# Performance work log

Measured on AMD Instinct MI355X. Metric: run time of the kernel, lower is better.

## Reference

```python
import jax, jax.numpy as jnp
import numpy as np

VOC = 32000; D = 512; DFF = 2048; L = 4; H = 8; DH = D // H
NN = 256; K = 8; NB = 32; R = 128; SMAX = 1024; B = 4; S = 1024
STD = 0.02


def _ln(x, s, b):
    m = x.mean(-1, keepdims=True)
    v = ((x - m) ** 2).mean(-1, keepdims=True)
    return (x - m) / jnp.sqrt(v + 1e-5) * s + b


def setup_inputs() -> dict:
    key = jax.random.key(0)
    ks = jax.random.split(key, 24)
    p = {}
    p["input_ids"] = jax.random.randint(ks[0], (B, S), 0, VOC)
    p["token_emb"] = jax.random.normal(ks[1], (VOC, D)) * STD
    p["pos_emb"] = jax.random.normal(ks[2], (SMAX, D)) * STD
    # fixed shared basis buffers (orthogonalized at init in torch; random stand-in, same forward math)
    bA = jax.random.normal(ks[3], (NB, D, R))
    p["basis_A"] = bA / jnp.linalg.norm(bA.reshape(NB, -1), axis=-1)[:, None, None]
    be = jax.random.normal(ks[4], (NB, D))
    p["basis_emb"] = be / jnp.linalg.norm(be, axis=-1, keepdims=True)
    # per-layer params stacked on leading L axis; torch Linear weight is [out, in]
    p["q_w"] = jax.random.normal(ks[5], (L, D, D)) * STD
    p["q_b"] = jnp.zeros((L, D))
    p["k_w"] = jax.random.normal(ks[6], (L, D, D)) * STD
    p["k_b"] = jnp.zeros((L, D))
    p["ao_w"] = jax.random.normal(ks[7], (L, D, D)) * STD
    p["ao_b"] = jnp.zeros((L, D))
    p["recipe"] = jax.random.normal(ks[8], (L, NN, NB)) * 0.5
    p["ctx_pat"] = jax.random.normal(ks[9], (L, NN, H)) * 0.5
    p["vout_w"] = jax.random.normal(ks[10], (L, D, R)) * STD
    p["vout_b"] = jnp.zeros((L, D))
    p["up_w"] = jax.random.normal(ks[11], (L, DFF, D)) * STD
    p["up_b"] = jnp.zeros((L, DFF))
    p["down_w"] = jax.random.normal(ks[12], (L, D, DFF)) * STD
    p["down_b"] = jnp.zeros((L, D))
    p["ln1_s"] = jnp.ones((L, D)); p["ln1_b"] = jnp.zeros((L, D))
    p["ln2_s"] = jnp.ones((L, D)); p["ln2_b"] = jnp.zeros((L, D))
    p["lnf_s"] = jnp.ones((D,)); p["lnf_b"] = jnp.zeros((D,))
    return p


def reference(input_ids, token_emb, pos_emb, basis_A, basis_emb,
              q_w, q_b, k_w, k_b, ao_w, ao_b, recipe, ctx_pat,
              vout_w, vout_b, up_w, up_b, down_w, down_b,
              ln1_s, ln1_b, ln2_s, ln2_b, lnf_s, lnf_b):
    Bb, Ss = input_ids.shape
    x = token_emb[input_ids] + pos_emb[:Ss][None]  # [B,S,D]
    causal = jnp.tril(jnp.ones((Ss, Ss), dtype=bool))
    scale = 1.0 / np.sqrt(DH)
    for l in range(L):
        normed = _ln(x, ln1_s[l], ln1_b[l])
        Q = (normed @ q_w[l].T + q_b[l]).reshape(Bb, Ss, H, DH).transpose(0, 2, 1, 3)
        Kk = (normed @ k_w[l].T + k_b[l]).reshape(Bb, Ss, H, DH).transpose(0, 2, 1, 3)
        scores = jnp.einsum('bhsd,bhtd->bhst', Q, Kk) * scale
        scores = jnp.where(causal, scores, -jnp.inf)
        attn = jax.nn.softmax(scores, axis=-1)  # [B,H,S,S]
        # --- neuron-based dynamic V ---
        rec_sm = jax.nn.softmax(recipe[l], axis=-1)        # [NN,NB]
        emb_sem = rec_sm @ basis_emb                        # [NN,D]
        sem = normed @ emb_sem.T                            # [B,S,NN]
        summary = attn.mean(-1).transpose(0, 2, 1)          # [B,S,H]
        ctx = summary @ ctx_pat[l].T                        # [B,S,NN]
        fin = sem * jax.nn.sigmoid(ctx)
        topv, idx = jax.lax.top_k(fin, K)                   # [B,S,K]
        w = jax.nn.softmax(topv, axis=-1)
        sel = jax.nn.softmax(recipe[l][idx], axis=-1)       # [B,S,K,NB]
        token_recipe = jnp.einsum('bskn,bsk->bsn', sel, w)  # [B,S,NB]
        # reassociated contraction (same math as bsn,ndr->bsdr then bsd,bsdr->bsr)
        xA = jnp.einsum('bsd,ndr->bsnr', normed, basis_A)   # [B,S,NB,R]
        v_sem = jnp.einsum('bsn,bsnr->bsr', token_recipe, xA)
        Vv = (v_sem @ vout_w[l].T + vout_b[l]).reshape(Bb, Ss, H, DH).transpose(0, 2, 1, 3)
        ao = jnp.einsum('bhst,bhtd->bhsd', attn, Vv).transpose(0, 2, 1, 3).reshape(Bb, Ss, D)
        x = x + ao @ ao_w[l].T + ao_b[l]
        normed2 = _ln(x, ln2_s[l], ln2_b[l])
        h = jax.nn.gelu(normed2 @ up_w[l].T + up_b[l], approximate=False)
        x = x + h @ down_w[l].T + down_b[l]
    x = _ln(x, lnf_s, lnf_b)
    return x @ token_emb.T  # tied head, [B,S,vocab]
```

## Files before the change

kernel.cpp:

```cpp
#include <hip/hip_runtime.h>
#include <hip/hip_bf16.h>
#include <math.h>

typedef __attribute__((ext_vector_type(8))) short short8;
typedef __attribute__((ext_vector_type(4))) short short4v;
typedef __attribute__((ext_vector_type(8))) __bf16 bf16x8;
typedef __attribute__((ext_vector_type(4))) float f32x4;
typedef unsigned short ushort;

#define DEVI static __device__ __forceinline__

DEVI ushort f2bf(float f) {
  union { float f; unsigned u; } v; v.f = f;
  unsigned r = v.u + 0x7fffu + ((v.u >> 16) & 1u);
  return (ushort)(r >> 16);
}
DEVI float bf2f(ushort h) {
  union { unsigned u; float f; } v; v.u = (unsigned)h << 16; return v.f;
}
DEVI void gload16(const void* g, void* l) {
  __builtin_amdgcn_global_load_lds((const __attribute__((address_space(1))) void*)g,
                                   (__attribute__((address_space(3))) void*)l, 16, 0, 0);
}

template<int BM, int EPI>
__global__ __launch_bounds__(256) void gemmT(
    const ushort* __restrict__ A, const ushort* __restrict__ B,
    void* __restrict__ Cv, const float* __restrict__ bias,
    int K, int lda, int ldb, int ldc, float scale)
{
  constexpr int MF = BM / 32;
  constexpr int MH = BM / 2;
  __shared__ ushort As[BM * 32];
  __shared__ ushort Bs[4096];

  const int gx = gridDim.x;
  const int nwg = gx * gridDim.y;
  const int orig = blockIdx.y * gx + blockIdx.x;
  const int q = nwg >> 3, r = nwg & 7;
  const int xcd = orig & 7, sidx = orig >> 3;
  const int wg = (xcd < r ? xcd * (q + 1) : r * (q + 1) + (xcd - r) * q) + sidx;
  const int n0 = (wg % gx) * 128, m0 = (wg / gx) * BM;

  const int tid = threadIdx.x;
  const int arow = tid >> 2, acolb = (tid & 3) << 4;
  const int lane = tid & 63, wv = tid >> 6;
  const int wm = wv >> 1, wn = wv & 1;
  const int l16 = lane & 15, lq = lane >> 4;

  f32x4 acc[MF][4];
#pragma unroll
  for (int i = 0; i < MF; i++)
#pragma unroll
    for (int j = 0; j < 4; j++) acc[i][j] = (f32x4){0.f, 0.f, 0.f, 0.f};

  const char* Ab = (const char*)(A + (long)(m0 + arow) * lda) + acolb;
  const char* Bb = (const char*)(B + (long)(n0 + arow) * ldb) + acolb;
  const long a64 = (long)64 * lda * 2, b64 = (long)64 * ldb * 2;
  char* la = (char*)As + tid * 16;
  char* lb = (char*)Bs + tid * 16;

  for (int k0 = 0; k0 < K; k0 += 32) {
    const char* ap = Ab + (long)k0 * 2;
    const char* bp = Bb + (long)k0 * 2;
#pragma unroll
    for (int s = 0; s < BM / 64; s++) gload16(ap + s * a64, la + s * 4096);
    gload16(bp, lb);
    gload16(bp + b64, lb + 4096);
    __syncthreads();
    bf16x8 af[MF], bfr[4];
#pragma unroll
    for (int i = 0; i < MF; i++)
      af[i] = __builtin_bit_cast(bf16x8, *(const short8*)&As[(wm*MH + i*16 + l16)*32 + lq*8]);
#pragma unroll
    for (int j = 0; j < 4; j++)
      bfr[j] = __builtin_bit_cast(bf16x8, *(const short8*)&Bs[(wn*64 + j*16 + l16)*32 + lq*8]);
#pragma unroll
    for (int i = 0; i < MF; i++)
#pragma unroll
      for (int j = 0; j < 4; j++)
        acc[i][j] = __builtin_amdgcn_mfma_f32_16x16x32_bf16(af[i], bfr[j], acc[i][j], 0, 0, 0);
    __syncthreads();
  }

  float* Cf = (float*)Cv;
  ushort* Ch = (ushort*)Cv;
#pragma unroll
  for (int i = 0; i < MF; i++) {
    const int row0 = m0 + wm*MH + i*16 + lq*4;
#pragma unroll
    for (int j = 0; j < 4; j++) {
      const int col = n0 + wn*64 + j*16 + l16;
      const float cb = bias ? bias[col] : 0.f;
#pragma unroll
      for (int t = 0; t < 4; t++) {
        float val = acc[i][j][t] * scale + cb;
        const long idx = (long)(row0 + t) * ldc + col;
        if (EPI == 1)      Ch[idx] = f2bf(val);
        else if (EPI == 2) { val = 0.5f * val * (1.f + erff(val * 0.70710678118654752f)); Ch[idx] = f2bf(val); }
        else if (EPI == 3) Cf[idx] += val;
        else               __builtin_nontemporal_store(val, Cf + idx);
      }
    }
  }
}

__global__ __launch_bounds__(256) void megag1(
    const ushort* __restrict__ A, const ushort* __restrict__ B,
    float* __restrict__ finb, ushort* __restrict__ qkh, ushort* __restrict__ XAb,
    const float* __restrict__ gate, const float* __restrict__ qkbias)
{
  __shared__ ushort As[4096];
  __shared__ ushort Bs[4096];
  const int gx = gridDim.x;
  const int nwg = gx * gridDim.y;
  const int orig = blockIdx.y * gx + blockIdx.x;
  const int q = nwg >> 3, r = nwg & 7;
  const int xcd = orig & 7, sidx = orig >> 3;
  const int wg = (xcd < r ? xcd * (q + 1) : r * (q + 1) + (xcd - r) * q) + sidx;
  const int n0 = (wg % gx) * 128, m0 = (wg / gx) * 128;

  const int tid = threadIdx.x;
  const int arow = tid >> 2, acolb = (tid & 3) << 4;
  const int lane = tid & 63, wv = tid >> 6;
  const int wm = wv >> 1, wn = wv & 1;
  const int l16 = lane & 15, lq = lane >> 4;

  f32x4 acc[4][4];
#pragma unroll
  for (int i = 0; i < 4; i++)
#pragma unroll
    for (int j = 0; j < 4; j++) acc[i][j] = (f32x4){0.f, 0.f, 0.f, 0.f};

  const char* Ab = (const char*)(A + (long)(m0 + arow) * 512) + acolb;
  const char* Bb = (const char*)(B + (long)(n0 + arow) * 512) + acolb;
  const long a64 = (long)64 * 512 * 2;
  char* la = (char*)As + tid * 16;
  char* lb = (char*)Bs + tid * 16;

  for (int k0 = 0; k0 < 512; k0 += 32) {
    const char* ap = Ab + (long)k0 * 2;
    const char* bp = Bb + (long)k0 * 2;
    gload16(ap, la);
    gload16(ap + a64, la + 4096);
    gload16(bp, lb);
    gload16(bp + a64, lb + 4096);
    __syncthreads();
    bf16x8 af[4], bfr[4];
#pragma unroll
    for (int i = 0; i < 4; i++) {
      af[i]  = __builtin_bit_cast(bf16x8, *(const short8*)&As[(wm*64 + i*16 + l16)*32 + lq*8]);
      bfr[i] = __builtin_bit_cast(bf16x8, *(const short8*)&Bs[(wn*64 + i*16 + l16)*32 + lq*8]);
    }
#pragma unroll
    for (int i = 0; i < 4; i++)
#pragma unroll
      for (int j = 0; j < 4; j++)
        acc[i][j] = __builtin_amdgcn_mfma_f32_16x16x32_bf16(af[i], bfr[j], acc[i][j], 0, 0, 0);
    __syncthreads();
  }

#pragma unroll
  for (int i = 0; i < 4; i++) {
    const int row0 = m0 + wm*64 + i*16 + lq*4;
#pragma unroll
    for (int j = 0; j < 4; j++) {
      const int col = n0 + wn*64 + j*16 + l16;
      if (col < 256) {
        const float g = gate[col];
#pragma unroll
        for (int t = 0; t < 4; t++) finb[(long)(row0 + t) * 256 + col] = acc[i][j][t] * g;
      } else if (col < 1280) {
        const int c = col - 256;
        const float bb = qkbias[c];
#pragma unroll
        for (int t = 0; t < 4; t++) qkh[(long)(row0 + t) * 1024 + c] = f2bf(acc[i][j][t] + bb);
      } else {
        const int c = col - 1280;
#pragma unroll
        for (int t = 0; t < 4; t++) XAb[(long)(row0 + t) * 4096 + c] = f2bf(acc[i][j][t]);
      }
    }
  }
}

__global__ __launch_bounds__(256) void flash_kernel(
    const ushort* __restrict__ qk, const ushort* __restrict__ v,
    ushort* __restrict__ o)
{
  __shared__ ushort Ks[4096];
  __shared__ ushort VTs[4096];
  __shared__ ushort Ps[4096];
  const int p = blockIdx.x, bh = blockIdx.y;
  const int b = bh >> 3, h = bh & 7;
  const int tid = threadIdx.x, lane = tid & 63, w = tid >> 6;
  const int l16 = lane & 15, lq = lane >> 4;
  const long tokbase = (long)b * 1024;
  const ushort* Qbase = qk + tokbase * 1024 + h * 64;
  const char*   Kbase = (const char*)(qk + tokbase * 1024 + 512 + h * 64);
  const ushort* Vbase = v + tokbase * 512 + h * 64;

  const int krow = tid >> 3, kcb = (tid & 7) << 4;
  const int vkv  = tid >> 2, vdb = (tid & 3) << 4;

#pragma unroll 1
  for (int half = 0; half < 2; half++) {
    const int qt = half ? (15 - p) : p;
    const int q0 = qt * 64;
    const int ntiles = qt + 1;

    const ushort* qrow = Qbase + (long)(q0 + w*16 + l16) * 1024;
    const bf16x8 qf0 = *(const bf16x8*)(qrow + lq*8);
    const bf16x8 qf1 = *(const bf16x8*)(qrow + 32 + lq*8);

    float m_[4] = {-1e30f, -1e30f, -1e30f, -1e30f};
    float l_[4] = {0.f, 0.f, 0.f, 0.f};
    f32x4 od[4];
#pragma unroll
    for (int dt = 0; dt < 4; dt++) od[dt] = (f32x4){0.f, 0.f, 0.f, 0.f};

#pragma unroll 1
    for (int t = 0; t < ntiles; t++) {
      const long t0 = (long)t * 64;
      {
        const int swz = kcb ^ ((krow & 7) << 4);
        gload16(Kbase + (t0 + krow) * 2048 + swz, (char*)Ks + tid * 16);
        gload16(Kbase + (t0 + 32 + krow) * 2048 + swz, (char*)Ks + 4096 + tid * 16);
      }
      {
        const ushort* vr = Vbase + (t0 + vkv) * 512 + vdb;
        short8 va = *(const short8*)vr;
        short8 vb = *(const short8*)(vr + 8);
#pragma unroll
        for (int j = 0; j < 8; j++) {
          int d1 = vdb + j, d2 = vdb + 8 + j;
          *(ushort*)((char*)VTs + d1*128 + ((vkv*2) ^ ((d1 & 7) << 4))) = (ushort)va[j];
          *(ushort*)((char*)VTs + d2*128 + ((vkv*2) ^ ((d2 & 7) << 4))) = (ushort)vb[j];
        }
      }
      __syncthreads();

      f32x4 sa[4];
#pragma unroll
      for (int n = 0; n < 4; n++) sa[n] = (f32x4){0.f, 0.f, 0.f, 0.f};
#pragma unroll
      for (int ks = 0; ks < 2; ks++) {
        const bf16x8 qf = ks ? qf1 : qf0;
#pragma unroll
        for (int n = 0; n < 4; n++) {
          const int row = n*16 + l16;
          bf16x8 kf = *(const bf16x8*)((const char*)Ks + row*128 + ((ks*64 + lq*16) ^ ((row & 7) << 4)));
          sa[n] = __builtin_amdgcn_mfma_f32_16x16x32_bf16(qf, kf, sa[n], 0, 0, 0);
        }
      }

      const bool diag = (t == qt);
      float rowmax[4] = {-1e30f, -1e30f, -1e30f, -1e30f};
#pragma unroll
      for (int n = 0; n < 4; n++)
#pragma unroll
        for (int r = 0; r < 4; r++) {
          float sv = sa[n][r] * 0.125f;
          if (diag && (n*16 + l16 > w*16 + lq*4 + r)) sv = -1e30f;
          sa[n][r] = sv;
          rowmax[r] = fmaxf(rowmax[r], sv);
        }
#pragma unroll
      for (int r = 0; r < 4; r++)
#pragma unroll
        for (int off = 8; off; off >>= 1) rowmax[r] = fmaxf(rowmax[r], __shfl_xor(rowmax[r], off));

      float psum[4];
#pragma unroll
      for (int r = 0; r < 4; r++) {
        const float mn = fmaxf(m_[r], rowmax[r]);
        const float corr = __expf(m_[r] - mn);
        m_[r] = mn;
        l_[r] *= corr;
#pragma unroll
        for (int dt = 0; dt < 4; dt++) od[dt][r] *= corr;
        psum[r] = 0.f;
      }
#pragma unroll
      for (int n = 0; n < 4; n++)
#pragma unroll
        for (int r = 0; r < 4; r++) {
          const float pv = __expf(sa[n][r] - m_[r]);
          psum[r] += pv;
          const int prow = w*16 + lq*4 + r;
          *(ushort*)((char*)Ps + prow*128 + (((n*16 + l16)*2) ^ ((prow & 7) << 4))) = f2bf(pv);
        }
#pragma unroll
      for (int r = 0; r < 4; r++) {
#pragma unroll
        for (int off = 8; off; off >>= 1) psum[r] += __shfl_xor(psum[r], off);
        l_[r] += psum[r];
      }

#pragma unroll
      for (int ks = 0; ks < 2; ks++) {
        const int prow = w*16 + l16;
        bf16x8 pf = *(const bf16x8*)((const char*)Ps + prow*128 + ((ks*64 + lq*16) ^ ((prow & 7) << 4)));
#pragma unroll
        for (int dt = 0; dt < 4; dt++) {
          const int vrow = dt*16 + l16;
          bf16x8 vf = *(const bf16x8*)((const char*)VTs + vrow*128 + ((ks*64 + lq*16) ^ ((vrow & 7) << 4)));
          od[dt] = __builtin_amdgcn_mfma_f32_16x16x32_bf16(pf, vf, od[dt], 0, 0, 0);
        }
      }
      __syncthreads();
    }

#pragma unroll
    for (int r = 0; r < 4; r++) {
      const float inv = 1.f / l_[r];
      ushort* orow = o + (tokbase + q0 + w*16 + lq*4 + r) * 512 + h * 64 + l16;
#pragma unroll
      for (int dt = 0; dt < 4; dt++) orow[dt*16] = f2bf(od[dt][r] * inv);
    }
  }
}

__global__ __launch_bounds__(256) void cvt_bf16(const float* __restrict__ src, ushort* __restrict__ dst) {
  long i = ((long)blockIdx.x * 256 + threadIdx.x) * 8;
  float4 u = *(const float4*)(src + i), v = *(const float4*)(src + i + 4);
  short8 s;
  s[0]=(short)f2bf(u.x); s[1]=(short)f2bf(u.y); s[2]=(short)f2bf(u.z); s[3]=(short)f2bf(u.w);
  s[4]=(short)f2bf(v.x); s[5]=(short)f2bf(v.y); s[6]=(short)f2bf(v.z); s[7]=(short)f2bf(v.w);
  *(short8*)(dst + i) = s;
}

__global__ __launch_bounds__(256) void qkcvt_kernel(
    const float* __restrict__ q_w, const float* __restrict__ k_w, ushort* __restrict__ Bcat)
{
  long e = ((long)blockIdx.x * 256 + threadIdx.x) * 8;
  int l = (int)(e >> 19);
  long rem = e & 524287;
  bool isk = rem >= 262144;
  long so = rem & 262143;
  const float* src = (isk ? k_w : q_w) + (long)l * 262144 + so;
  ushort* dst = Bcat + (long)l * 2752512 + 131072 + (isk ? 262144 : 0) + so;
  float4 u = *(const float4*)src, v = *(const float4*)(src + 4);
  short8 s;
  s[0]=(short)f2bf(u.x); s[1]=(short)f2bf(u.y); s[2]=(short)f2bf(u.z); s[3]=(short)f2bf(u.w);
  s[4]=(short)f2bf(v.x); s[5]=(short)f2bf(v.y); s[6]=(short)f2bf(v.z); s[7]=(short)f2bf(v.w);
  *(short8*)dst = s;
}

__global__ __launch_bounds__(256) void mkqkb_kernel(const float* __restrict__ qb,
    const float* __restrict__ kb, float* __restrict__ qkb) {
  int i = blockIdx.x * 256 + threadIdx.x;
  int l = i >> 10, c = i & 1023;
  qkb[i] = c < 512 ? qb[l*512 + c] : kb[l*512 + c - 512];
}

__global__ __launch_bounds__(256) void transpose_basisA(
    const float* __restrict__ src, ushort* __restrict__ Bcat)
{
  __shared__ ushort tile[64][132];
  const int n = blockIdx.x;
  const int d0 = blockIdx.y * 64;
  const int l = blockIdx.z;
  ushort* dst = Bcat + (long)l * 2752512 + 655360;
  const int tid = threadIdx.x;
#pragma unroll
  for (int it = 0; it < 8; it++) {
    int d = it * 8 + (tid >> 5);
    int rr = (tid & 31) * 4;
    float4 v = *(const float4*)(src + ((long)n * 512 + d0 + d) * 128 + rr);
    tile[d][rr + 0] = f2bf(v.x);
    tile[d][rr + 1] = f2bf(v.y);
    tile[d][rr + 2] = f2bf(v.z);
    tile[d][rr + 3] = f2bf(v.w);
  }
  __syncthreads();
#pragma unroll
  for (int it = 0; it < 4; it++) {
    int rr = it * 32 + (tid >> 3);
    int dof = (tid & 7) * 8;
    short8 s;
#pragma unroll
    for (int j = 0; j < 8; j++) s[j] = (short)tile[dof + j][rr];
    *(short8*)(dst + ((long)n * 128 + rr) * 512 + d0 + dof) = s;
  }
}

__global__ __launch_bounds__(256) void embed_kernel(
    const int* __restrict__ ids, const float* __restrict__ tok,
    const float* __restrict__ pos, float* __restrict__ x)
{
  int i = blockIdx.x * 256 + threadIdx.x;
  int t = i >> 7, c = (i & 127) * 4;
  int sp = t & 1023;
  int id = ids[t];
  float4 a = *(const float4*)(tok + (long)id * 512 + c);
  float4 b = *(const float4*)(pos + (long)sp * 512 + c);
  float4 rr; rr.x=a.x+b.x; rr.y=a.y+b.y; rr.z=a.z+b.z; rr.w=a.w+b.w;
  *(float4*)(x + (long)t * 512 + c) = rr;
}

__global__ __launch_bounds__(256) void ln_kernel(
    const float* __restrict__ in, ushort* __restrict__ outh,
    const float* __restrict__ gam, const float* __restrict__ bet)
{
  int row = blockIdx.x * 4 + (threadIdx.x >> 6);
  int lane = threadIdx.x & 63;
  const float* p = in + (long)row * 512;
  float4 v0 = *(const float4*)(p + lane * 4);
  float4 v1 = *(const float4*)(p + 256 + lane * 4);
  float s = v0.x+v0.y+v0.z+v0.w + v1.x+v1.y+v1.z+v1.w;
#pragma unroll
  for (int o = 32; o; o >>= 1) s += __shfl_xor(s, o);
  float mean = s * (1.f/512.f);
  float d0=v0.x-mean, d1=v0.y-mean, d2=v0.z-mean, d3=v0.w-mean;
  float e0=v1.x-mean, e1=v1.y-mean, e2=v1.z-mean, e3=v1.w-mean;
  float qv = d0*d0+d1*d1+d2*d2+d3*d3 + e0*e0+e1*e1+e2*e2+e3*e3;
#pragma unroll
  for (int o = 32; o; o >>= 1) qv += __shfl_xor(qv, o);
  float inv = rsqrtf(qv * (1.f/512.f) + 1e-5f);
  float4 g0 = *(const float4*)(gam + lane*4);
  float4 g1 = *(const float4*)(gam + 256 + lane*4);
  float4 b0 = *(const float4*)(bet + lane*4);
  float4 b1 = *(const float4*)(bet + 256 + lane*4);
  short4v o0, o1;
  o0[0]=(short)f2bf(d0*inv*g0.x + b0.x); o0[1]=(short)f2bf(d1*inv*g0.y + b0.y);
  o0[2]=(short)f2bf(d2*inv*g0.z + b0.z); o0[3]=(short)f2bf(d3*inv*g0.w + b0.w);
  o1[0]=(short)f2bf(e0*inv*g1.x + b1.x); o1[1]=(short)f2bf(e1*inv*g1.y + b1.y);
  o1[2]=(short)f2bf(e2*inv*g1.z + b1.z); o1[3]=(short)f2bf(e3*inv*g1.w + b1.w);
  *(short4v*)(outh + (long)row*512 + lane*4) = o0;
  *(short4v*)(outh + (long)row*512 + 256 + lane*4) = o1;
}

__global__ __launch_bounds__(64) void precompute_kernel(
    const float* __restrict__ recipe, const float* __restrict__ basis_emb,
    const float* __restrict__ ctx_pat, float* __restrict__ rec_sm,
    ushort* __restrict__ Bcat, float* __restrict__ gate)
{
  int ln = blockIdx.x;
  int l = ln >> 8, n = ln & 255;
  int lane = threadIdx.x;
  const float* r = recipe + (long)ln * 32;
  float rv[32];
  float m = -1e30f;
#pragma unroll
  for (int j = 0; j < 32; j++) { rv[j] = r[j]; m = fmaxf(m, rv[j]); }
  float sum = 0.f;
#pragma unroll
  for (int j = 0; j < 32; j++) { rv[j] = expf(rv[j] - m); sum += rv[j]; }
  float inv = 1.f / sum;
#pragma unroll
  for (int j = 0; j < 32; j++) rv[j] *= inv;
  if (lane < 32) rec_sm[(long)ln * 32 + lane] = rv[lane];
  ushort* dst = Bcat + (long)l * 2752512 + (long)n * 512;
#pragma unroll
  for (int cc = 0; cc < 8; cc++) {
    int c = lane + cc * 64;
    float acc = 0.f;
#pragma unroll
    for (int j = 0; j < 32; j++) acc += rv[j] * basis_emb[j * 512 + c];
    dst[c] = f2bf(acc);
  }
  if (lane == 0) {
    float sh = 0.f;
#pragma unroll
    for (int h = 0; h < 8; h++) sh += ctx_pat[(long)ln * 8 + h];
    gate[ln] = 1.f / (1.f + expf(-sh * (1.f/1024.f)));
  }
}

__global__ __launch_bounds__(256) void topkvsem_kernel(
    const float* __restrict__ fin, const float* __restrict__ rec_sm_l,
    const ushort* __restrict__ XA, ushort* __restrict__ out)
{
  __shared__ float trs[4][32];
  int wv = threadIdx.x >> 6, lane = threadIdx.x & 63;
  int t = blockIdx.x * 4 + wv;
  const float* f = fin + (long)t * 256;
  float v0 = f[lane], v1 = f[lane+64], v2 = f[lane+128], v3 = f[lane+192];
  int i0 = lane, i1 = lane+64, i2 = lane+128, i3 = lane+192;
  float topv[8]; int topi[8];
#pragma unroll
  for (int it = 0; it < 8; it++) {
    float bm = v0; int bi = i0;
    if (v1 > bm || (v1 == bm && i1 < bi)) { bm = v1; bi = i1; }
    if (v2 > bm || (v2 == bm && i2 < bi)) { bm = v2; bi = i2; }
    if (v3 > bm || (v3 == bm && i3 < bi)) { bm = v3; bi = i3; }
#pragma unroll
    for (int o = 32; o; o >>= 1) {
      float om = __shfl_xor(bm, o);
      int oi = __shfl_xor(bi, o);
      if (om > bm || (om == bm && oi < bi)) { bm = om; bi = oi; }
    }
    topv[it] = bm; topi[it] = bi;
    if (i0 == bi) v0 = -1e30f;
    if (i1 == bi) v1 = -1e30f;
    if (i2 == bi) v2 = -1e30f;
    if (i3 == bi) v3 = -1e30f;
  }
  float w[8], wsum = 0.f;
#pragma unroll
  for (int k = 0; k < 8; k++) { w[k] = expf(topv[k] - topv[0]); wsum += w[k]; }
  float winv = 1.f / wsum;
  if (lane < 32) {
    float acc = 0.f;
#pragma unroll
    for (int k = 0; k < 8; k++)
      acc += (w[k] * winv) * rec_sm_l[(long)topi[k] * 32 + lane];
    trs[wv][lane] = acc;
  }
  __syncthreads();
  const ushort* xa = XA + (long)t * 4096;
  float a0 = 0.f, a1 = 0.f;
#pragma unroll
  for (int n = 0; n < 32; n++) {
    float wn = trs[wv][n];
    a0 += wn * bf2f(xa[n*128 + lane]);
    a1 += wn * bf2f(xa[n*128 + 64 + lane]);
  }
  out[(long)t * 128 + lane] = f2bf(a0);
  out[(long)t * 128 + 64 + lane] = f2bf(a1);
}

extern "C" void kernel_launch(void* const* d_in, const int* in_sizes, int n_in,
                              void* d_out, int out_size, void* d_ws, size_t ws_size,
                              hipStream_t stream) {
  (void)in_sizes; (void)n_in; (void)out_size; (void)ws_size;
  const int*   ids       = (const int*)  d_in[0];
  const float* token_emb = (const float*)d_in[1];
  const float* pos_emb   = (const float*)d_in[2];
  const float* basis_A   = (const float*)d_in[3];
  const float* basis_emb = (const float*)d_in[4];
  const float* q_w  = (const float*)d_in[5];
  const float* q_b  = (const float*)d_in[6];
  const float* k_w  = (const float*)d_in[7];
  const float* k_b  = (const float*)d_in[8];
  const float* ao_w = (const float*)d_in[9];
  const float* ao_b = (const float*)d_in[10];
  const float* recipe  = (const float*)d_in[11];
  const float* ctx_pat = (const float*)d_in[12];
  const float* vout_w  = (const float*)d_in[13];
  const float* vout_b  = (const float*)d_in[14];
  const float* up_w    = (const float*)d_in[15];
  const float* up_b    = (const float*)d_in[16];
  const float* down_w  = (const float*)d_in[17];
  const float* down_b  = (const float*)d_in[18];
  const float* ln1_s = (const float*)d_in[19];
  const float* ln1_b = (const float*)d_in[20];
  const float* ln2_s = (const float*)d_in[21];
  const float* ln2_b = (const float*)d_in[22];
  const float* lnf_s = (const float*)d_in[23];
  const float* lnf_b = (const float*)d_in[24];
  float* out = (float*)d_out;

  float* ws    = (float*)d_ws;
  float* x     = ws;
  float* finb  = x + 2097152;
  float* recsm = finb + 1048576;
  float* gate  = recsm + 32768;
  float* qkb   = gate + 1024;
  ushort* u = (ushort*)(qkb + 4096);
  ushort* nrmh    = u; u += 2097152;
  ushort* vsemh   = u; u += 524288;
  ushort* Bcat    = u; u += 11010048;
  ushort* aowh    = u; u += 1048576;
  ushort* voutwh  = u; u += 262144;
  ushort* upwh    = u; u += 4194304;
  ushort* downwh  = u; u += 4194304;
  ushort* tembh   = u; u += 16384000;

  ushort* XAb = (ushort*)out;
  ushort* HF  = (ushort*)out;
  ushort* qkh = (ushort*)out + 16777216;
  ushort* vvh = (ushort*)out + 20971520;
  ushort* aoh = (ushort*)out + 23068672;

  qkcvt_kernel<<<1024, 256, 0, stream>>>(q_w, k_w, Bcat);
  mkqkb_kernel<<<16, 256, 0, stream>>>(q_b, k_b, qkb);
  cvt_bf16<<<512, 256, 0, stream>>>(ao_w, aowh);
  cvt_bf16<<<128, 256, 0, stream>>>(vout_w, voutwh);
  cvt_bf16<<<2048, 256, 0, stream>>>(up_w, upwh);
  cvt_bf16<<<2048, 256, 0, stream>>>(down_w, downwh);
  cvt_bf16<<<8000, 256, 0, stream>>>(token_emb, tembh);
  transpose_basisA<<<dim3(32, 8, 4), 256, 0, stream>>>(basis_A, Bcat);
  embed_kernel<<<2048, 256, 0, stream>>>(ids, token_emb, pos_emb, x);
  precompute_kernel<<<1024, 64, 0, stream>>>(recipe, basis_emb, ctx_pat, recsm, Bcat, gate);

  for (int l = 0; l < 4; l++) {
    ln_kernel<<<1024, 256, 0, stream>>>(x, nrmh, ln1_s + l*512, ln1_b + l*512);
    megag1<<<dim3(42, 32), 256, 0, stream>>>(nrmh, Bcat + (long)l*2752512,
        finb, qkh, XAb, gate + l*256, qkb + l*1024);
    topkvsem_kernel<<<1024, 256, 0, stream>>>(finb, recsm + (long)l*8192, XAb, vsemh);
    gemmT<64,1><<<dim3(4, 64), 256, 0, stream>>>(vsemh, voutwh + (long)l*65536, vvh,
        vout_b + l*512, 128, 128, 128, 512, 1.f);
    flash_kernel<<<dim3(8, 32), 256, 0, stream>>>(qkh, vvh, aoh);
    gemmT<64,3><<<dim3(4, 64), 256, 0, stream>>>(aoh, aowh + (long)l*262144, x,
        ao_b + l*512, 512, 512, 512, 512, 1.f);
    ln_kernel<<<1024, 256, 0, stream>>>(x, nrmh, ln2_s + l*512, ln2_b + l*512);
    gemmT<128,2><<<dim3(16, 32), 256, 0, stream>>>(nrmh, upwh + (long)l*1048576, (void*)HF,
        up_b + l*2048, 512, 512, 512, 2048, 1.f);
    gemmT<64,3><<<dim3(4, 64), 256, 0, stream>>>(HF, downwh + (long)l*1048576, x,
        down_b + l*512, 2048, 2048, 2048, 512, 1.f);
  }

  ln_kernel<<<1024, 256, 0, stream>>>(x, nrmh, lnf_s, lnf_b);
  gemmT<128,4><<<dim3(250, 32), 256, 0, stream>>>(nrmh, tembh, out, nullptr,
      512, 512, 512, 32000, 1.f);
}
```

Measured before the change: 1.133 ms.

## Deepen GEMM K-tiles, double-buffer flash K/V, fuse conversions and embed+LN

Raises the GEMM and megag1 K-tile from 32 to 64 so each barrier pair covers two MFMA k-steps, halving the synchronisation count. The flash kernel double-buffers its K and transposed V tiles in shared memory, issuing the next tile's loads before the current tile's compute. The separate weight-conversion launches are merged into one cvt_all kernel, and the embedding add is fused with the first layer norm. Together these cut launch overhead and hide load latency, at the cost of more LDS per block, which may reduce occupancy.

```diff
diff --git a/kernel.cpp b/kernel.cpp
--- a/kernel.cpp
+++ b/kernel.cpp
@@ -29,21 +29,23 @@
     void* __restrict__ Cv, const float* __restrict__ bias,
     int K, int lda, int ldb, int ldc, float scale)
 {
+  constexpr int BK = 64;
   constexpr int MF = BM / 32;
   constexpr int MH = BM / 2;
-  __shared__ ushort As[BM * 32];
-  __shared__ ushort Bs[4096];
+  constexpr int ACH = BM * BK / 2048;
+  constexpr int BCH = 128 * BK / 2048;
+  __shared__ ushort As[BM * BK];
+  __shared__ ushort Bs[128 * BK];
 
   const int gx = gridDim.x;
   const int nwg = gx * gridDim.y;
   const int orig = blockIdx.y * gx + blockIdx.x;
-  const int q = nwg >> 3, r = nwg & 7;
+  const int qq = nwg >> 3, rr = nwg & 7;
   const int xcd = orig & 7, sidx = orig >> 3;
-  const int wg = (xcd < r ? xcd * (q + 1) : r * (q + 1) + (xcd - r) * q) + sidx;
+  const int wg = (xcd < rr ? xcd * (qq + 1) : rr * (qq + 1) + (xcd - rr) * qq) + sidx;
   const int n0 = (wg % gx) * 128, m0 = (wg / gx) * BM;
 
   const int tid = threadIdx.x;
-  const int arow = tid >> 2, acolb = (tid & 3) << 4;
   const int lane = tid & 63, wv = tid >> 6;
   const int wm = wv >> 1, wn = wv & 1;
   const int l16 = lane & 15, lq = lane >> 4;
@@ -54,32 +56,40 @@
 #pragma unroll
     for (int j = 0; j < 4; j++) acc[i][j] = (f32x4){0.f, 0.f, 0.f, 0.f};
 
-  const char* Ab = (const char*)(A + (long)(m0 + arow) * lda) + acolb;
-  const char* Bb = (const char*)(B + (long)(n0 + arow) * ldb) + acolb;
-  const long a64 = (long)64 * lda * 2, b64 = (long)64 * ldb * 2;
-  char* la = (char*)As + tid * 16;
-  char* lb = (char*)Bs + tid * 16;
-
-  for (int k0 = 0; k0 < K; k0 += 32) {
-    const char* ap = Ab + (long)k0 * 2;
-    const char* bp = Bb + (long)k0 * 2;
-#pragma unroll
-    for (int s = 0; s < BM / 64; s++) gload16(ap + s * a64, la + s * 4096);
-    gload16(bp, lb);
-    gload16(bp + b64, lb + 4096);
+  const char* apS[ACH]; const char* bpS[BCH];
+#pragma unroll
+  for (int s = 0; s < ACH; s++) {
+    int c = tid + 256 * s;
+    apS[s] = (const char*)(A + (long)(m0 + (c >> 3)) * lda) + ((c & 7) << 4);
+  }
+#pragma unroll
+  for (int s = 0; s < BCH; s++) {
+    int c = tid + 256 * s;
+    bpS[s] = (const char*)(B + (long)(n0 + (c >> 3)) * ldb) + ((c & 7) << 4);
+  }
+
+  for (int k0 = 0; k0 < K; k0 += BK) {
+    const long kb = (long)k0 * 2;
+#pragma unroll
+    for (int s = 0; s < ACH; s++) gload16(apS[s] + kb, (char*)As + (tid + 256*s) * 16);
+#pragma unroll
+    for (int s = 0; s < BCH; s++) gload16(bpS[s] + kb, (char*)Bs + (tid + 256*s) * 16);
     __syncthreads();
-    bf16x8 af[MF], bfr[4];
-#pragma unroll
-    for (int i = 0; i < MF; i++)
-      af[i] = __builtin_bit_cast(bf16x8, *(const short8*)&As[(wm*MH + i*16 + l16)*32 + lq*8]);
-#pragma unroll
-    for (int j = 0; j < 4; j++)
-      bfr[j] = __builtin_bit_cast(bf16x8, *(const short8*)&Bs[(wn*64 + j*16 + l16)*32 + lq*8]);
-#pragma unroll
-    for (int i = 0; i < MF; i++)
+#pragma unroll
+    for (int ks = 0; ks < 2; ks++) {
+      bf16x8 af[MF], bfr[4];
+#pragma unroll
+      for (int i = 0; i < MF; i++)
+        af[i] = __builtin_bit_cast(bf16x8, *(const short8*)&As[(wm*MH + i*16 + l16)*BK + ks*32 + lq*8]);
 #pragma unroll
       for (int j = 0; j < 4; j++)
-        acc[i][j] = __builtin_amdgcn_mfma_f32_16x16x32_bf16(af[i], bfr[j], acc[i][j], 0, 0, 0);
+        bfr[j] = __builtin_bit_cast(bf16x8, *(const short8*)&Bs[(wn*64 + j*16 + l16)*BK + ks*32 + lq*8]);
+#pragma unroll
+      for (int i = 0; i < MF; i++)
+#pragma unroll
+        for (int j = 0; j < 4; j++)
+          acc[i][j] = __builtin_amdgcn_mfma_f32_16x16x32_bf16(af[i], bfr[j], acc[i][j], 0, 0, 0);
+    }
     __syncthreads();
   }
 
@@ -110,18 +120,18 @@
     float* __restrict__ finb, ushort* __restrict__ qkh, ushort* __restrict__ XAb,
     const float* __restrict__ gate, const float* __restrict__ qkbias)
 {
-  __shared__ ushort As[4096];
-  __shared__ ushort Bs[4096];
+  constexpr int BK = 64;
+  __shared__ ushort As[128 * BK];
+  __shared__ ushort Bs[128 * BK];
   const int gx = gridDim.x;
   const int nwg = gx * gridDim.y;
   const int orig = blockIdx.y * gx + blockIdx.x;
-  const int q = nwg >> 3, r = nwg & 7;
+  const int qq = nwg >> 3, rr = nwg & 7;
   const int xcd = orig & 7, sidx = orig >> 3;
-  const int wg = (xcd < r ? xcd * (q + 1) : r * (q + 1) + (xcd - r) * q) + sidx;
+  const int wg = (xcd < rr ? xcd * (qq + 1) : rr * (qq + 1) + (xcd - rr) * qq) + sidx;
   const int n0 = (wg % gx) * 128, m0 = (wg / gx) * 128;
 
   const int tid = threadIdx.x;
-  const int arow = tid >> 2, acolb = (tid & 3) << 4;
   const int lane = tid & 63, wv = tid >> 6;
   const int wm = wv >> 1, wn = wv & 1;
   const int l16 = lane & 15, lq = lane >> 4;
@@ -132,31 +142,36 @@
 #pragma unroll
     for (int j = 0; j < 4; j++) acc[i][j] = (f32x4){0.f, 0.f, 0.f, 0.f};
 
-  const char* Ab = (const char*)(A + (long)(m0 + arow) * 512) + acolb;
-  const char* Bb = (const char*)(B + (long)(n0 + arow) * 512) + acolb;
-  const long a64 = (long)64 * 512 * 2;
-  char* la = (char*)As + tid * 16;
-  char* lb = (char*)Bs + tid * 16;
-
-  for (int k0 = 0; k0 < 512; k0 += 32) {
-    const char* ap = Ab + (long)k0 * 2;
-    const char* bp = Bb + (long)k0 * 2;
-    gload16(ap, la);
-    gload16(ap + a64, la + 4096);
-    gload16(bp, lb);
-    gload16(bp + a64, lb + 4096);
+  const char* apS[4]; const char* bpS[4];
+#pragma unroll
+  for (int s = 0; s < 4; s++) {
+    int c = tid + 256 * s;
+    apS[s] = (const char*)(A + (long)(m0 + (c >> 3)) * 512) + ((c & 7) << 4);
+    bpS[s] = (const char*)(B + (long)(n0 + (c >> 3)) * 512) + ((c & 7) << 4);
+  }
+
+  for (int k0 = 0; k0 < 512; k0 += BK) {
+    const long kb = (long)k0 * 2;
+#pragma unroll
+    for (int s = 0; s < 4; s++) {
+      gload16(apS[s] + kb, (char*)As + (tid + 256*s) * 16);
+      gload16(bpS[s] + kb, (char*)Bs + (tid + 256*s) * 16);
+    }
     __syncthreads();
-    bf16x8 af[4], bfr[4];
-#pragma unroll
-    for (int i = 0; i < 4; i++) {
-      af[i]  = __builtin_bit_cast(bf16x8, *(const short8*)&As[(wm*64 + i*16 + l16)*32 + lq*8]);
-      bfr[i] = __builtin_bit_cast(bf16x8, *(const short8*)&Bs[(wn*64 + i*16 + l16)*32 + lq*8]);
-    }
-#pragma unroll
-    for (int i = 0; i < 4; i++)
-#pragma unroll
-      for (int j = 0; j < 4; j++)
-        acc[i][j] = __builtin_amdgcn_mfma_f32_16x16x32_bf16(af[i], bfr[j], acc[i][j], 0, 0, 0);
+#pragma unroll
+    for (int ks = 0; ks < 2; ks++) {
+      bf16x8 af[4], bfr[4];
+#pragma unroll
+      for (int i = 0; i < 4; i++) {
+        af[i]  = __builtin_bit_cast(bf16x8, *(const short8*)&As[(wm*64 + i*16 + l16)*BK + ks*32 + lq*8]);
+        bfr[i] = __builtin_bit_cast(bf16x8, *(const short8*)&Bs[(wn*64 + i*16 + l16)*BK + ks*32 + lq*8]);
+      }
+#pragma unroll
+      for (int i = 0; i < 4; i++)
+#pragma unroll
+        for (int j = 0; j < 4; j++)
+          acc[i][j] = __builtin_amdgcn_mfma_f32_16x16x32_bf16(af[i], bfr[j], acc[i][j], 0, 0, 0);
+    }
     __syncthreads();
   }
 
@@ -188,8 +203,8 @@
     const ushort* __restrict__ qk, const ushort* __restrict__ v,
     ushort* __restrict__ o)
 {
-  __shared__ ushort Ks[4096];
-  __shared__ ushort VTs[4096];
+  __shared__ ushort Ks[2][4096];
+  __shared__ ushort VTs[2][4096];
   __shared__ ushort Ps[4096];
   const int p = blockIdx.x, bh = blockIdx.y;
   const int b = bh >> 3, h = bh & 7;
@@ -202,6 +217,7 @@
 
   const int krow = tid >> 3, kcb = (tid & 7) << 4;
   const int vkv  = tid >> 2, vdb = (tid & 3) << 4;
+  const int kswz = kcb ^ ((krow & 7) << 4);
 
 #pragma unroll 1
   for (int half = 0; half < 2; half++) {
@@ -219,26 +235,34 @@
 #pragma unroll
     for (int dt = 0; dt < 4; dt++) od[dt] = (f32x4){0.f, 0.f, 0.f, 0.f};
 
+    gload16(Kbase + (long)krow * 2048 + kswz, (char*)Ks[0] + tid * 16);
+    gload16(Kbase + (long)(32 + krow) * 2048 + kswz, (char*)Ks[0] + 4096 + tid * 16);
+    {
+      const ushort* vr = Vbase + (long)vkv * 512 + vdb;
+      short8 va = *(const short8*)vr;
+      short8 vb = *(const short8*)(vr + 8);
+#pragma unroll
+      for (int j = 0; j < 8; j++) {
+        int d1 = vdb + j, d2 = vdb + 8 + j;
+        *(ushort*)((char*)VTs[0] + d1*128 + ((vkv*2) ^ ((d1 & 7) << 4))) = (ushort)va[j];
+        *(ushort*)((char*)VTs[0] + d2*128 + ((vkv*2) ^ ((d2 & 7) << 4))) = (ushort)vb[j];
+      }
+    }
+    __syncthreads();
+
+    int cur = 0;
 #pragma unroll 1
     for (int t = 0; t < ntiles; t++) {
-      const long t0 = (long)t * 64;
-      {
-        const int swz = kcb ^ ((krow & 7) << 4);
-        gload16(Kbase + (t0 + krow) * 2048 + swz, (char*)Ks + tid * 16);
-        gload16(Kbase + (t0 + 32 + krow) * 2048 + swz, (char*)Ks + 4096 + tid * 16);
-      }
-      {
-        const ushort* vr = Vbase + (t0 + vkv) * 512 + vdb;
-        short8 va = *(const short8*)vr;
-        short8 vb = *(const short8*)(vr + 8);
-#pragma unroll
-        for (int j = 0; j < 8; j++) {
-          int d1 = vdb + j, d2 = vdb + 8 + j;
-          *(ushort*)((char*)VTs + d1*128 + ((vkv*2) ^ ((d1 & 7) << 4))) = (ushort)va[j];
-          *(ushort*)((char*)VTs + d2*128 + ((vkv*2) ^ ((d2 & 7) << 4))) = (ushort)vb[j];
-        }
-      }
-      __syncthreads();
+      const bool hasn = (t + 1 < ntiles);
+      short8 vaN, vbN;
+      if (hasn) {
+        const long n0g = (long)(t + 1) * 64;
+        gload16(Kbase + (n0g + krow) * 2048 + kswz, (char*)Ks[cur ^ 1] + tid * 16);
+        gload16(Kbase + (n0g + 32 + krow) * 2048 + kswz, (char*)Ks[cur ^ 1] + 4096 + tid * 16);
+        const ushort* vr = Vbase + (n0g + vkv) * 512 + vdb;
+        vaN = *(const short8*)vr;
+        vbN = *(const short8*)(vr + 8);
+      }
 
       f32x4 sa[4];
 #pragma unroll
@@ -249,7 +273,7 @@
 #pragma unroll
         for (int n = 0; n < 4; n++) {
           const int row = n*16 + l16;
-          bf16x8 kf = *(const bf16x8*)((const char*)Ks + row*128 + ((ks*64 + lq*16) ^ ((row & 7) << 4)));
+          bf16x8 kf = *(const bf16x8*)((const char*)Ks[cur] + row*128 + ((ks*64 + lq*16) ^ ((row & 7) << 4)));
           sa[n] = __builtin_amdgcn_mfma_f32_16x16x32_bf16(qf, kf, sa[n], 0, 0, 0);
         }
       }
@@ -304,11 +328,21 @@
 #pragma unroll
         for (int dt = 0; dt < 4; dt++) {
           const int vrow = dt*16 + l16;
-          bf16x8 vf = *(const bf16x8*)((const char*)VTs + vrow*128 + ((ks*64 + lq*16) ^ ((vrow & 7) << 4)));
+          bf16x8 vf = *(const bf16x8*)((const char*)VTs[cur] + vrow*128 + ((ks*64 + lq*16) ^ ((vrow & 7) << 4)));
           od[dt] = __builtin_amdgcn_mfma_f32_16x16x32_bf16(pf, vf, od[dt], 0, 0, 0);
         }
       }
+
+      if (hasn) {
+#pragma unroll
+        for (int j = 0; j < 8; j++) {
+          int d1 = vdb + j, d2 = vdb + 8 + j;
+          *(ushort*)((char*)VTs[cur ^ 1] + d1*128 + ((vkv*2) ^ ((d1 & 7) << 4))) = (ushort)vaN[j];
+          *(ushort*)((char*)VTs[cur ^ 1] + d2*128 + ((vkv*2) ^ ((d2 & 7) << 4))) = (ushort)vbN[j];
+        }
+      }
       __syncthreads();
+      cur ^= 1;
     }
 
 #pragma unroll
@@ -321,37 +355,53 @@
   }
 }
 
-__global__ __launch_bounds__(256) void cvt_bf16(const float* __restrict__ src, ushort* __restrict__ dst) {
-  long i = ((long)blockIdx.x * 256 + threadIdx.x) * 8;
-  float4 u = *(const float4*)(src + i), v = *(const float4*)(src + i + 4);
-  short8 s;
-  s[0]=(short)f2bf(u.x); s[1]=(short)f2bf(u.y); s[2]=(short)f2bf(u.z); s[3]=(short)f2bf(u.w);
-  s[4]=(short)f2bf(v.x); s[5]=(short)f2bf(v.y); s[6]=(short)f2bf(v.z); s[7]=(short)f2bf(v.w);
-  *(short8*)(dst + i) = s;
-}
-
-__global__ __launch_bounds__(256) void qkcvt_kernel(
-    const float* __restrict__ q_w, const float* __restrict__ k_w, ushort* __restrict__ Bcat)
-{
-  long e = ((long)blockIdx.x * 256 + threadIdx.x) * 8;
-  int l = (int)(e >> 19);
-  long rem = e & 524287;
-  bool isk = rem >= 262144;
-  long so = rem & 262143;
-  const float* src = (isk ? k_w : q_w) + (long)l * 262144 + so;
-  ushort* dst = Bcat + (long)l * 2752512 + 131072 + (isk ? 262144 : 0) + so;
-  float4 u = *(const float4*)src, v = *(const float4*)(src + 4);
-  short8 s;
-  s[0]=(short)f2bf(u.x); s[1]=(short)f2bf(u.y); s[2]=(short)f2bf(u.z); s[3]=(short)f2bf(u.w);
-  s[4]=(short)f2bf(v.x); s[5]=(short)f2bf(v.y); s[6]=(short)f2bf(v.z); s[7]=(short)f2bf(v.w);
-  *(short8*)dst = s;
-}
-
-__global__ __launch_bounds__(256) void mkqkb_kernel(const float* __restrict__ qb,
-    const float* __restrict__ kb, float* __restrict__ qkb) {
-  int i = blockIdx.x * 256 + threadIdx.x;
-  int l = i >> 10, c = i & 1023;
-  qkb[i] = c < 512 ? qb[l*512 + c] : kb[l*512 + c - 512];
+DEVI void cvt8(const float* s, ushort* d) {
+  float4 u = *(const float4*)s, v = *(const float4*)(s + 4);
+  short8 o;
+  o[0]=(short)f2bf(u.x); o[1]=(short)f2bf(u.y); o[2]=(short)f2bf(u.z); o[3]=(short)f2bf(u.w);
+  o[4]=(short)f2bf(v.x); o[5]=(short)f2bf(v.y); o[6]=(short)f2bf(v.z); o[7]=(short)f2bf(v.w);
+  *(short8*)d = o;
+}
+__global__ __launch_bounds__(256) void cvt_all(
+    const float* __restrict__ q_w, const float* __restrict__ k_w,
+    const float* __restrict__ ao_w, const float* __restrict__ vout_w,
+    const float* __restrict__ up_w, const float* __restrict__ down_w,
+    const float* __restrict__ temb, const float* __restrict__ q_b,
+    const float* __restrict__ k_b,
+    ushort* __restrict__ Bcat, ushort* __restrict__ aowh, ushort* __restrict__ voutwh,
+    ushort* __restrict__ upwh, ushort* __restrict__ downwh, ushort* __restrict__ tembh,
+    float* __restrict__ qkb)
+{
+  long u = (long)blockIdx.x * 256 + threadIdx.x;
+  if (u < 262144) {
+    long e = u * 8;
+    int l = (int)(e >> 19);
+    long rem = e & 524287;
+    bool isk = rem >= 262144;
+    long so = rem & 262143;
+    cvt8((isk ? k_w : q_w) + (long)l * 262144 + so,
+         Bcat + (long)l * 2752512 + 131072 + (isk ? 262144 : 0) + so);
+    return;
+  }
+  u -= 262144;
+  if (u < 131072) { cvt8(ao_w + u*8, aowh + u*8); return; }
+  u -= 131072;
+  if (u < 32768)  { cvt8(vout_w + u*8, voutwh + u*8); return; }
+  u -= 32768;
+  if (u < 524288) { cvt8(up_w + u*8, upwh + u*8); return; }
+  u -= 524288;
+  if (u < 524288) { cvt8(down_w + u*8, downwh + u*8); return; }
+  u -= 524288;
+  if (u < 2048000){ cvt8(temb + u*8, tembh + u*8); return; }
+  u -= 2048000;
+  {
+    long i8 = u * 8;
+    int l = (int)(i8 >> 10), c = (int)(i8 & 1023);
+    const float* src = (c < 512) ? (q_b + l*512 + c) : (k_b + l*512 + c - 512);
+    float* dst = qkb + i8;
+    *(float4*)dst = *(const float4*)src;
+    *(float4*)(dst + 4) = *(const float4*)(src + 4);
+  }
 }
 
 __global__ __launch_bounds__(256) void transpose_basisA(
@@ -385,18 +435,45 @@
   }
 }
 
-__global__ __launch_bounds__(256) void embed_kernel(
+__global__ __launch_bounds__(256) void embed_ln(
     const int* __restrict__ ids, const float* __restrict__ tok,
-    const float* __restrict__ pos, float* __restrict__ x)
-{
-  int i = blockIdx.x * 256 + threadIdx.x;
-  int t = i >> 7, c = (i & 127) * 4;
-  int sp = t & 1023;
-  int id = ids[t];
-  float4 a = *(const float4*)(tok + (long)id * 512 + c);
-  float4 b = *(const float4*)(pos + (long)sp * 512 + c);
-  float4 rr; rr.x=a.x+b.x; rr.y=a.y+b.y; rr.z=a.z+b.z; rr.w=a.w+b.w;
-  *(float4*)(x + (long)t * 512 + c) = rr;
+    const float* __restrict__ pos, const float* __restrict__ gam,
+    const float* __restrict__ bet, float* __restrict__ x, ushort* __restrict__ outh)
+{
+  int row = blockIdx.x * 4 + (threadIdx.x >> 6);
+  int lane = threadIdx.x & 63;
+  int id = ids[row], sp = row & 1023;
+  const float* tp = tok + (long)id * 512;
+  const float* pp = pos + (long)sp * 512;
+  float4 v0 = *(const float4*)(tp + lane*4);
+  float4 p0 = *(const float4*)(pp + lane*4);
+  float4 v1 = *(const float4*)(tp + 256 + lane*4);
+  float4 p1 = *(const float4*)(pp + 256 + lane*4);
+  v0.x+=p0.x; v0.y+=p0.y; v0.z+=p0.z; v0.w+=p0.w;
+  v1.x+=p1.x; v1.y+=p1.y; v1.z+=p1.z; v1.w+=p1.w;
+  *(float4*)(x + (long)row*512 + lane*4) = v0;
+  *(float4*)(x + (long)row*512 + 256 + lane*4) = v1;
+  float s = v0.x+v0.y+v0.z+v0.w + v1.x+v1.y+v1.z+v1.w;
+#pragma unroll
+  for (int o = 32; o; o >>= 1) s += __shfl_xor(s, o);
+  float mean = s * (1.f/512.f);
+  float d0=v0.x-mean, d1=v0.y-mean, d2=v0.z-mean, d3=v0.w-mean;
+  float e0=v1.x-mean, e1=v1.y-mean, e2=v1.z-mean, e3=v1.w-mean;
+  float qv = d0*d0+d1*d1+d2*d2+d3*d3 + e0*e0+e1*e1+e2*e2+e3*e3;
+#pragma unroll
+  for (int o = 32; o; o >>= 1) qv += __shfl_xor(qv, o);
+  float inv = rsqrtf(qv * (1.f/512.f) + 1e-5f);
+  float4 g0 = *(const float4*)(gam + lane*4);
+  float4 g1 = *(const float4*)(gam + 256 + lane*4);
+  float4 b0 = *(const float4*)(bet + lane*4);
+  float4 b1 = *(const float4*)(bet + 256 + lane*4);
+  short4v o0, o1;
+  o0[0]=(short)f2bf(d0*inv*g0.x + b0.x); o0[1]=(short)f2bf(d1*inv*g0.y + b0.y);
+  o0[2]=(short)f2bf(d2*inv*g0.z + b0.z); o0[3]=(short)f2bf(d3*inv*g0.w + b0.w);
+  o1[0]=(short)f2bf(e0*inv*g1.x + b1.x); o1[1]=(short)f2bf(e1*inv*g1.y + b1.y);
+  o1[2]=(short)f2bf(e2*inv*g1.z + b1.z); o1[3]=(short)f2bf(e3*inv*g1.w + b1.w);
+  *(short4v*)(outh + (long)row*512 + lane*4) = o0;
+  *(short4v*)(outh + (long)row*512 + 256 + lane*4) = o1;
 }
 
 __global__ __launch_bounds__(256) void ln_kernel(
@@ -574,19 +651,14 @@
   ushort* vvh = (ushort*)out + 20971520;
   ushort* aoh = (ushort*)out + 23068672;
 
-  qkcvt_kernel<<<1024, 256, 0, stream>>>(q_w, k_w, Bcat);
-  mkqkb_kernel<<<16, 256, 0, stream>>>(q_b, k_b, qkb);
-  cvt_bf16<<<512, 256, 0, stream>>>(ao_w, aowh);
-  cvt_bf16<<<128, 256, 0, stream>>>(vout_w, voutwh);
-  cvt_bf16<<<2048, 256, 0, stream>>>(up_w, upwh);
-  cvt_bf16<<<2048, 256, 0, stream>>>(down_w, downwh);
-  cvt_bf16<<<8000, 256, 0, stream>>>(token_emb, tembh);
+  cvt_all<<<13762, 256, 0, stream>>>(q_w, k_w, ao_w, vout_w, up_w, down_w,
+      token_emb, q_b, k_b, Bcat, aowh, voutwh, upwh, downwh, tembh, qkb);
   transpose_basisA<<<dim3(32, 8, 4), 256, 0, stream>>>(basis_A, Bcat);
-  embed_kernel<<<2048, 256, 0, stream>>>(ids, token_emb, pos_emb, x);
   precompute_kernel<<<1024, 64, 0, stream>>>(recipe, basis_emb, ctx_pat, recsm, Bcat, gate);
+  embed_ln<<<1024, 256, 0, stream>>>(ids, token_emb, pos_emb, ln1_s, ln1_b, x, nrmh);
 
   for (int l = 0; l < 4; l++) {
-    ln_kernel<<<1024, 256, 0, stream>>>(x, nrmh, ln1_s + l*512, ln1_b + l*512);
+    if (l) ln_kernel<<<1024, 256, 0, stream>>>(x, nrmh, ln1_s + l*512, ln1_b + l*512);
     megag1<<<dim3(42, 32), 256, 0, stream>>>(nrmh, Bcat + (long)l*2752512,
         finb, qkh, XAb, gate + l*256, qkb + l*1024);
     topkvsem_kernel<<<1024, 256, 0, stream>>>(finb, recsm + (long)l*8192, XAb, vsemh);
```

Result: no change. 1.132 ms (-0.1%).
